# Optimization experiments

Hardware: AMD Instinct MI355X
Metric: run time of the kernel (lower is better)

## Reference

```python
import jax, jax.numpy as jnp
import numpy as np

B, S, H, E = 32, 4096, 512, 512

def setup_inputs() -> dict:
    key = jax.random.key(0)
    ks = jax.random.split(key, 11)
    sc = 1.0 / np.sqrt(H)
    return {
        "context": jax.random.normal(ks[0], (B, S, H), jnp.float32),
        "h": jax.random.normal(ks[1], (B, H), jnp.float32),
        "x": jax.random.normal(ks[2], (B, E), jnp.float32),
        "We": jax.random.normal(ks[3], (H, H), jnp.float32) * sc,
        "be": jax.random.normal(ks[4], (H,), jnp.float32) * sc,
        "Wd": jax.random.normal(ks[5], (H, H), jnp.float32) * sc,
        "bd": jax.random.normal(ks[6], (H,), jnp.float32) * sc,
        "Wv": jax.random.normal(ks[7], (H,), jnp.float32) * sc,
        "bv": jax.random.normal(ks[8], (1,), jnp.float32) * sc,
        "Wr": jax.random.normal(ks[9], (2 * H, 2 * H + E), jnp.float32) * (1.0 / np.sqrt(2 * H + E)),
        "br": jax.random.normal(ks[10], (2 * H,), jnp.float32) * sc,
    }

def reference(context, h, x, We, be, Wd, bd, Wv, bv, Wr, br):
    # gamma_encoder: [B,S,H]; gamma_decoder: [B,1,H]
    ge = jnp.einsum('bsh,kh->bsk', context, We) + be
    gd = h @ Wd.T + bd
    # additive scores -> [B,S]
    scores = jnp.einsum('bsh,h->bs', jnp.tanh(ge + gd[:, None, :]), Wv) + bv[0]
    weights = jax.nn.softmax(scores, axis=1)
    # context vector c_t: [B,H]
    c_t = jnp.einsum('bs,bsh->bh', weights, context)
    # linear_r on [c_t, h, x] -> [B,2H]
    r_t = jnp.concatenate([c_t, h, x], axis=1) @ Wr.T + br
    # maxout over pairs: view [B,H,2].max(-1)
    output = jnp.max(r_t.reshape(-1, r_t.shape[1] // 2, 2), axis=2)
    return (output, weights)
```

## Files before the change

### kernel.cpp

```cpp
#include <hip/hip_runtime.h>

typedef __attribute__((ext_vector_type(8))) short bf16x8;
typedef __attribute__((ext_vector_type(16))) float f32x16;

typedef __attribute__((address_space(3))) unsigned int lds_u32;
typedef __attribute__((address_space(1))) unsigned int glb_u32;

__device__ inline unsigned int cvt_pk_bf16(float lo, float hi){
  unsigned int r;
  asm("v_cvt_pk_bf16_f32 %0, %1, %2" : "=v"(r) : "v"(lo), "v"(hi));
  return r;
}
__device__ inline bf16x8 pack8(float4 a, float4 b){
  union { unsigned int u[4]; bf16x8 v; } r;
  r.u[0]=cvt_pk_bf16(a.x,a.y); r.u[1]=cvt_pk_bf16(a.z,a.w);
  r.u[2]=cvt_pk_bf16(b.x,b.y); r.u[3]=cvt_pk_bf16(b.z,b.w);
  return r.v;
}
__device__ inline float fast_tanh(float x){
  float e = __builtin_amdgcn_exp2f(x * 2.8853900817779268f);
  return 1.0f - 2.0f * __builtin_amdgcn_rcpf(e + 1.0f);
}

__global__ __launch_bounds__(256) void we_conv(const float* __restrict__ We,
                                               uint4* __restrict__ weFrag){
  int gid = blockIdx.x * 256 + threadIdx.x;
  int l  = gid & 63;
  int hc = gid >> 10;
  int colv = (hc >> 1)*32 + (l & 31);
  int k = ((hc & 1) << 8) + ((gid >> 6) & 15)*16 + (l >> 5)*8;
  const float4* src = (const float4*)(We + colv*512 + k);
  float4 f0 = src[0], f1 = src[1];
  weFrag[gid] = make_uint4(cvt_pk_bf16(f0.x,f0.y), cvt_pk_bf16(f0.z,f0.w),
                           cvt_pk_bf16(f1.x,f1.y), cvt_pk_bf16(f1.z,f1.w));
}

__global__ __launch_bounds__(256) void gd_kernel(const float* __restrict__ hvec,
                                                 const float* __restrict__ Wd,
                                                 const float* __restrict__ bd,
                                                 const float* __restrict__ be,
                                                 float* __restrict__ gd){
  __shared__ float hs[512];
  int b = blockIdx.x >> 2, kc = blockIdx.x & 3;
  int tid = threadIdx.x;
  hs[tid]       = hvec[b*512 + tid];
  hs[tid + 256] = hvec[b*512 + 256 + tid];
  __syncthreads();
  int k  = kc*128 + (tid >> 1);
  int hh = (tid & 1) * 256;
  const float4* wrow = (const float4*)(Wd + (size_t)k*512 + hh);
  const float4* hv4  = (const float4*)(hs + hh);
  float acc = 0.f;
  #pragma unroll 8
  for (int i = 0; i < 64; ++i){
    float4 w = wrow[i]; float4 u = hv4[i];
    acc += w.x*u.x + w.y*u.y + w.z*u.z + w.w*u.w;
  }
  acc += __shfl_xor(acc, 1);
  if ((tid & 1) == 0) gd[b*512 + k] = acc + bd[k] + be[k];
}

__global__ __launch_bounds__(256, 2) void score_kernel(
    const float* __restrict__ ctx, const char* __restrict__ weFrag,
    const float* __restrict__ gd, const float* __restrict__ Wv,
    float* __restrict__ scores){
  __shared__ char lds[3*16384 + 4096];
  float* gdwv = (float*)(lds + 49152);

  const int tid  = threadIdx.x;
  const int wid  = tid >> 6;
  const int lane = tid & 63;
  const int bid  = blockIdx.x;
  const int row0 = bid * 128;
  const int b    = bid >> 5;
  const int col  = lane & 31;
  const int hi   = lane >> 5;

  if (tid < 128) ((float4*)gdwv)[tid] = ((const float4*)(gd + b*512))[tid];
  else           ((float4*)gdwv)[tid] = ((const float4*)Wv)[tid - 128];

  bf16x8 afrag[32];
  {
    const float4* ap = (const float4*)(ctx + (size_t)(row0 + wid*32 + col)*512 + hi*8);
    #pragma unroll
    for (int t = 0; t < 32; ++t)
      afrag[t] = pack8(ap[t*4], ap[t*4 + 1]);
  }

  asm volatile("s_waitcnt lgkmcnt(0)" ::: "memory");

  #define ISSUE(HC, BUF) do { \
    const char* _g = weFrag + ((size_t)(HC))*16384 + wid*4096; \
    char* _l = lds + (BUF)*16384 + wid*4096; \
    _Pragma("unroll") \
    for (int _i = 0; _i < 4; ++_i) \
      __builtin_amdgcn_global_load_lds((const glb_u32*)(_g + _i*1024 + lane*16), \
                                       (lds_u32*)(_l + _i*1024), 16, 0, 0); \
  } while(0)

  ISSUE(0, 0);
  ISSUE(1, 1);

  f32x16 acc;
  float sc[16];
  #pragma unroll
  for (int r = 0; r < 16; ++r) sc[r] = 0.f;

  for (int nc = 0; nc < 16; ++nc){
    const int hc0 = 2*nc, hc1 = 2*nc + 1;

    asm volatile("s_waitcnt vmcnt(4)" ::: "memory");
    __builtin_amdgcn_s_barrier();
    if (hc0 < 30) ISSUE(hc0 + 2, (hc0 + 2) % 3);
    {
      const char* bb = lds + (hc0 % 3)*16384 + lane*16;
      #pragma unroll
      for (int r = 0; r < 16; ++r) acc[r] = 0.f;
      __builtin_amdgcn_s_setprio(1);
      #pragma unroll
      for (int t = 0; t < 16; ++t){
        bf16x8 bf = *(const bf16x8*)(bb + t*1024);
        acc = __builtin_amdgcn_mfma_f32_32x32x16_bf16(afrag[t], bf, acc, 0, 0, 0);
      }
      __builtin_amdgcn_s_setprio(0);
    }

    if (nc < 15) asm volatile("s_waitcnt vmcnt(4)" ::: "memory");
    else         asm volatile("s_waitcnt vmcnt(0)" ::: "memory");
    __builtin_amdgcn_s_barrier();
    if (hc1 < 30) ISSUE(hc1 + 2, (hc1 + 2) % 3);
    {
      const char* bb = lds + (hc1 % 3)*16384 + lane*16;
      __builtin_amdgcn_s_setprio(1);
      #pragma unroll
      for (int t = 0; t < 16; ++t){
        bf16x8 bf = *(const bf16x8*)(bb + t*1024);
        acc = __builtin_amdgcn_mfma_f32_32x32x16_bf16(afrag[16 + t], bf, acc, 0, 0, 0);
      }
      __builtin_amdgcn_s_setprio(0);
    }

    {
      float gdv = gdwv[nc*32 + col];
      float wvv = gdwv[512 + nc*32 + col];
      #pragma unroll
      for (int r = 0; r < 16; ++r)
        sc[r] += fast_tanh(acc[r] + gdv) * wvv;
    }
  }
  #undef ISSUE

  #pragma unroll
  for (int r = 0; r < 16; ++r){
    #pragma unroll
    for (int m = 1; m <= 16; m <<= 1) sc[r] += __shfl_xor(sc[r], m);
  }
  if (col == 0){
    float* so = scores + row0 + wid*32 + 4*hi;
    #pragma unroll
    for (int r = 0; r < 16; ++r)
      so[(r & 3) + 8*(r >> 2)] = sc[r];
  }
}

__global__ __launch_bounds__(256) void softmax_kernel(const float* __restrict__ scores,
                                                      float* __restrict__ weights){
  __shared__ float red[8];
  int b = blockIdx.x, tid = threadIdx.x;
  const float4* src = (const float4*)(scores + b*4096);
  float4* dst = (float4*)(weights + b*4096);
  float4 v[4];
  float m = -1e30f;
  #pragma unroll
  for (int i = 0; i < 4; ++i){
    v[i] = src[tid + i*256];
    m = fmaxf(m, fmaxf(fmaxf(v[i].x, v[i].y), fmaxf(v[i].z, v[i].w)));
  }
  #pragma unroll
  for (int o = 1; o < 64; o <<= 1) m = fmaxf(m, __shfl_xor(m, o));
  if ((tid & 63) == 0) red[tid >> 6] = m;
  __syncthreads();
  m = fmaxf(fmaxf(red[0], red[1]), fmaxf(red[2], red[3]));
  float s = 0.f;
  #pragma unroll
  for (int i = 0; i < 4; ++i){
    v[i].x = __builtin_amdgcn_exp2f((v[i].x - m) * 1.4426950408889634f);
    v[i].y = __builtin_amdgcn_exp2f((v[i].y - m) * 1.4426950408889634f);
    v[i].z = __builtin_amdgcn_exp2f((v[i].z - m) * 1.4426950408889634f);
    v[i].w = __builtin_amdgcn_exp2f((v[i].w - m) * 1.4426950408889634f);
    s += v[i].x + v[i].y + v[i].z + v[i].w;
  }
  #pragma unroll
  for (int o = 1; o < 64; o <<= 1) s += __shfl_xor(s, o);
  if ((tid & 63) == 0) red[4 + (tid >> 6)] = s;
  __syncthreads();
  s = red[4] + red[5] + red[6] + red[7];
  float inv = 1.0f / s;
  #pragma unroll
  for (int i = 0; i < 4; ++i){
    v[i].x *= inv; v[i].y *= inv; v[i].z *= inv; v[i].w *= inv;
    dst[tid + i*256] = v[i];
  }
}

__global__ __launch_bounds__(256) void ct_partial(const float* __restrict__ ctx,
                                                  const float* __restrict__ wbuf,
                                                  float* __restrict__ part){
  int bid = blockIdx.x;
  int b = bid >> 4, ch = bid & 15;
  int tid = threadIdx.x;
  int hq = tid & 127;
  int sh = tid >> 7;
  const float* wrow = wbuf + b*4096 + ch*256;
  const float4* src = (const float4*)(ctx + ((size_t)b*4096 + (size_t)ch*256)*512) + hq;
  float4 acc = {0.f,0.f,0.f,0.f};
  #pragma unroll 8
  for (int s = sh; s < 256; s += 2){
    float w = wrow[s];
    float4 c = src[(size_t)s*128];
    acc.x += w*c.x; acc.y += w*c.y; acc.z += w*c.z; acc.w += w*c.w;
  }
  ((float4*)(part + (size_t)bid*1024 + sh*512))[hq] = acc;
}

__global__ __launch_bounds__(128) void ct_reduce(const float* __restrict__ part,
                                                 float* __restrict__ ct){
  int b = blockIdx.x, tid = threadIdx.x;
  const float4* p = (const float4*)(part + (size_t)b*16384) + tid;
  float4 acc = {0.f,0.f,0.f,0.f};
  #pragma unroll
  for (int g = 0; g < 32; ++g){
    float4 v = p[g*128];
    acc.x += v.x; acc.y += v.y; acc.z += v.z; acc.w += v.w;
  }
  ((float4*)(ct + b*512))[tid] = acc;
}

__global__ __launch_bounds__(256) void final_kernel(
    const float* __restrict__ ct, const float* __restrict__ hvec,
    const float* __restrict__ x, const float* __restrict__ Wr,
    const float* __restrict__ br, float* __restrict__ out){
  __shared__ float xs[8][1536];
  int bt = blockIdx.x >> 4;
  int it = blockIdx.x & 15;
  int tid = threadIdx.x;
  int b0 = bt * 8;
  for (int idx = tid; idx < 8*1536; idx += 256){
    int bl = idx / 1536, j = idx % 1536;
    int b = b0 + bl;
    float v = (j < 512) ? ct[b*512 + j]
            : (j < 1024) ? hvec[b*512 + (j - 512)]
            : x[b*512 + (j - 1024)];
    xs[bl][j] = v;
  }
  __syncthreads();
  int i = it*64 + (tid & 63);
  int bl0 = (tid >> 6) * 2;
  const float4* wrow = (const float4*)(Wr + (size_t)i*1536);
  const float4* x0 = (const float4*)xs[bl0];
  const float4* x1 = (const float4*)xs[bl0 + 1];
  float a0 = 0.f, a1 = 0.f;
  #pragma unroll 4
  for (int k = 0; k < 384; ++k){
    float4 w = wrow[k];
    float4 u0 = x0[k], u1 = x1[k];
    a0 += w.x*u0.x + w.y*u0.y + w.z*u0.z + w.w*u0.w;
    a1 += w.x*u1.x + w.y*u1.y + w.z*u1.z + w.w*u1.w;
  }
  float bias = br[i];
  a0 += bias; a1 += bias;
  float n0 = __shfl_xor(a0, 1);
  float n1 = __shfl_xor(a1, 1);
  if ((tid & 1) == 0){
    out[(b0 + bl0    )*512 + (i >> 1)] = fmaxf(a0, n0);
    out[(b0 + bl0 + 1)*512 + (i >> 1)] = fmaxf(a1, n1);
  }
}

extern "C" void kernel_launch(void* const* d_in, const int* in_sizes, int n_in,
                              void* d_out, int out_size, void* d_ws, size_t ws_size,
                              hipStream_t stream){
  const float* ctx  = (const float*)d_in[0];
  const float* hvec = (const float*)d_in[1];
  const float* x    = (const float*)d_in[2];
  const float* We   = (const float*)d_in[3];
  const float* be   = (const float*)d_in[4];
  const float* Wd   = (const float*)d_in[5];
  const float* bd   = (const float*)d_in[6];
  const float* Wv   = (const float*)d_in[7];
  const float* Wr   = (const float*)d_in[9];
  const float* br   = (const float*)d_in[10];

  float* out     = (float*)d_out;
  float* weights = out + 32*512;

  char* ws = (char*)d_ws;
  char* weFrag  = ws;
  float* scores = (float*)(ws + (512 << 10));
  float* part   = (float*)(ws + (1024 << 10));
  float* ct     = (float*)(ws + (3 << 20));
  float* gd     = (float*)(ws + (3 << 20) + (64 << 10));

  we_conv<<<128, 256, 0, stream>>>(We, (uint4*)weFrag);
  gd_kernel<<<128, 256, 0, stream>>>(hvec, Wd, bd, be, gd);
  score_kernel<<<1024, 256, 0, stream>>>(ctx, weFrag, gd, Wv, scores);
  softmax_kernel<<<32, 256, 0, stream>>>(scores, weights);
  ct_partial<<<512, 256, 0, stream>>>(ctx, weights, part);
  ct_reduce<<<32, 128, 0, stream>>>(part, ct);
  final_kernel<<<64, 256, 0, stream>>>(ct, hvec, x, Wr, br, out);
}
```

Measured before the change: 219.6 us.

## Load We fragments directly into registers instead of LDS triple buffering

Measured after the change: 248.9 us. 1.13x slower.

```diff
diff --git a/kernel.cpp b/kernel.cpp
--- a/kernel.cpp
+++ b/kernel.cpp
@@ -2,9 +2,6 @@
 
 typedef __attribute__((ext_vector_type(8))) short bf16x8;
 typedef __attribute__((ext_vector_type(16))) float f32x16;
-
-typedef __attribute__((address_space(3))) unsigned int lds_u32;
-typedef __attribute__((address_space(1))) unsigned int glb_u32;
 
 __device__ inline unsigned int cvt_pk_bf16(float lo, float hi){
   unsigned int r;
@@ -60,13 +57,10 @@
   if ((tid & 1) == 0) gd[b*512 + k] = acc + bd[k] + be[k];
 }
 
-__global__ __launch_bounds__(256, 2) void score_kernel(
-    const float* __restrict__ ctx, const char* __restrict__ weFrag,
+__global__ __launch_bounds__(256) void score_kernel(
+    const float* __restrict__ ctx, const uint4* __restrict__ weFrag,
     const float* __restrict__ gd, const float* __restrict__ Wv,
     float* __restrict__ scores){
-  __shared__ char lds[3*16384 + 4096];
-  float* gdwv = (float*)(lds + 49152);
-
   const int tid  = threadIdx.x;
   const int wid  = tid >> 6;
   const int lane = tid & 63;
@@ -76,9 +70,6 @@
   const int col  = lane & 31;
   const int hi   = lane >> 5;
 
-  if (tid < 128) ((float4*)gdwv)[tid] = ((const float4*)(gd + b*512))[tid];
-  else           ((float4*)gdwv)[tid] = ((const float4*)Wv)[tid - 128];
-
   bf16x8 afrag[32];
   {
     const float4* ap = (const float4*)(ctx + (size_t)(row0 + wid*32 + col)*512 + hi*8);
@@ -87,68 +78,50 @@
       afrag[t] = pack8(ap[t*4], ap[t*4 + 1]);
   }
 
-  asm volatile("s_waitcnt lgkmcnt(0)" ::: "memory");
-
-  #define ISSUE(HC, BUF) do { \
-    const char* _g = weFrag + ((size_t)(HC))*16384 + wid*4096; \
-    char* _l = lds + (BUF)*16384 + wid*4096; \
+  const float* gdp = gd + b*512;
+
+  #define LOADH(DST, HC) do { \
+    const uint4* _p = weFrag + ((HC)*16)*64 + lane; \
     _Pragma("unroll") \
-    for (int _i = 0; _i < 4; ++_i) \
-      __builtin_amdgcn_global_load_lds((const glb_u32*)(_g + _i*1024 + lane*16), \
-                                       (lds_u32*)(_l + _i*1024), 16, 0, 0); \
+    for (int _i = 0; _i < 16; ++_i) \
+      *(uint4*)&DST[_i] = _p[_i*64]; \
   } while(0)
 
-  ISSUE(0, 0);
-  ISSUE(1, 1);
-
-  f32x16 acc;
+  bf16x8 bA[16], bB[16];
+  LOADH(bA, 0);
+
   float sc[16];
   #pragma unroll
   for (int r = 0; r < 16; ++r) sc[r] = 0.f;
 
   for (int nc = 0; nc < 16; ++nc){
-    const int hc0 = 2*nc, hc1 = 2*nc + 1;
-
-    asm volatile("s_waitcnt vmcnt(4)" ::: "memory");
-    __builtin_amdgcn_s_barrier();
-    if (hc0 < 30) ISSUE(hc0 + 2, (hc0 + 2) % 3);
-    {
-      const char* bb = lds + (hc0 % 3)*16384 + lane*16;
-      #pragma unroll
-      for (int r = 0; r < 16; ++r) acc[r] = 0.f;
-      __builtin_amdgcn_s_setprio(1);
-      #pragma unroll
-      for (int t = 0; t < 16; ++t){
-        bf16x8 bf = *(const bf16x8*)(bb + t*1024);
-        acc = __builtin_amdgcn_mfma_f32_32x32x16_bf16(afrag[t], bf, acc, 0, 0, 0);
-      }
-      __builtin_amdgcn_s_setprio(0);
-    }
-
-    if (nc < 15) asm volatile("s_waitcnt vmcnt(4)" ::: "memory");
-    else         asm volatile("s_waitcnt vmcnt(0)" ::: "memory");
-    __builtin_amdgcn_s_barrier();
-    if (hc1 < 30) ISSUE(hc1 + 2, (hc1 + 2) % 3);
-    {
-      const char* bb = lds + (hc1 % 3)*16384 + lane*16;
-      __builtin_amdgcn_s_setprio(1);
-      #pragma unroll
-      for (int t = 0; t < 16; ++t){
-        bf16x8 bf = *(const bf16x8*)(bb + t*1024);
-        acc = __builtin_amdgcn_mfma_f32_32x32x16_bf16(afrag[16 + t], bf, acc, 0, 0, 0);
-      }
-      __builtin_amdgcn_s_setprio(0);
-    }
-
-    {
-      float gdv = gdwv[nc*32 + col];
-      float wvv = gdwv[512 + nc*32 + col];
-      #pragma unroll
-      for (int r = 0; r < 16; ++r)
-        sc[r] += fast_tanh(acc[r] + gdv) * wvv;
-    }
-  }
-  #undef ISSUE
+    LOADH(bB, 2*nc + 1);
+
+    f32x16 accLo, accHi;
+    #pragma unroll
+    for (int r = 0; r < 16; ++r){ accLo[r] = 0.f; accHi[r] = 0.f; }
+
+    __builtin_amdgcn_s_setprio(1);
+    #pragma unroll
+    for (int t = 0; t < 16; ++t)
+      accLo = __builtin_amdgcn_mfma_f32_32x32x16_bf16(afrag[t], bA[t], accLo, 0, 0, 0);
+    __builtin_amdgcn_s_setprio(0);
+
+    if (nc < 15) LOADH(bA, 2*nc + 2);
+
+    __builtin_amdgcn_s_setprio(1);
+    #pragma unroll
+    for (int t = 0; t < 16; ++t)
+      accHi = __builtin_amdgcn_mfma_f32_32x32x16_bf16(afrag[16 + t], bB[t], accHi, 0, 0, 0);
+    __builtin_amdgcn_s_setprio(0);
+
+    float gdv = gdp[nc*32 + col];
+    float wvv = Wv[nc*32 + col];
+    #pragma unroll
+    for (int r = 0; r < 16; ++r)
+      sc[r] += fast_tanh(accLo[r] + accHi[r] + gdv) * wvv;
+  }
+  #undef LOADH
 
   #pragma unroll
   for (int r = 0; r < 16; ++r){
@@ -303,7 +276,7 @@
 
   we_conv<<<128, 256, 0, stream>>>(We, (uint4*)weFrag);
   gd_kernel<<<128, 256, 0, stream>>>(hvec, Wd, bd, be, gd);
-  score_kernel<<<1024, 256, 0, stream>>>(ctx, weFrag, gd, Wv, scores);
+  score_kernel<<<1024, 256, 0, stream>>>(ctx, (const uint4*)weFrag, gd, Wv, scores);
   softmax_kernel<<<32, 256, 0, stream>>>(scores, weights);
   ct_partial<<<512, 256, 0, stream>>>(ctx, weights, part);
   ct_reduce<<<32, 128, 0, stream>>>(part, ct);
```
